# Performance work log

Hardware: AMD Instinct MI355X
Metric: run time of the kernel (lower is better)

The kernel has to match this reference:

```python
import jax, jax.numpy as jnp
import numpy as np

REG_MAX = 16
NUM_CLASSES = 30
IMG_SIZE = 320.0


def make_anchors(strides=(8, 16, 32), feats_shapes=((40, 40), (20, 20), (10, 10))):
    pts = []
    for stride, (h, w) in zip(strides, feats_shapes):
        sx = np.arange(w, dtype=np.float32) + 0.5
        sy = np.arange(h, dtype=np.float32) + 0.5
        gy, gx = np.meshgrid(sy, sx, indexing='ij')
        pts.append(np.stack((gx, gy), -1).reshape(-1, 2) * stride)
    return jnp.asarray(np.concatenate(pts, 0))  # [2100, 2]


def setup_inputs() -> dict:
    key = jax.random.key(0)
    k1, k2, k3, k4 = jax.random.split(key, 4)
    B, M = 128, 50
    pred = jax.random.normal(k1, (B, 4 * REG_MAX + NUM_CLASSES, 2100), dtype=jnp.float32)
    targets_cls = jax.random.randint(k2, (B, M), 0, NUM_CLASSES, dtype=jnp.int32)
    targets_xy = jax.random.uniform(k3, (B, M, 2), dtype=jnp.float32)  # normalized centers
    valid = jax.random.randint(k4, (B, M), 0, 2) > 0  # bool GT-validity mask
    anchors = make_anchors()
    return {"pred": pred, "targets_cls": targets_cls, "targets_xy": targets_xy,
            "valid": valid, "anchors": anchors}


def reference(pred, targets_cls, targets_xy, valid, anchors):
    B = pred.shape[0]
    A = anchors.shape[0]  # 2100
    pred_dist = pred[:, :4 * REG_MAX, :]   # [B, 64, A]
    pred_cls = pred[:, 4 * REG_MAX:, :]    # [B, C, A]

    # --- vectorized nearest-anchor assignment (replaces nested python loops) ---
    centers = targets_xy * IMG_SIZE                               # [B, M, 2]
    dist = jnp.linalg.norm(anchors[None, None, :, :] - centers[:, :, None, :], axis=-1)  # [B, M, A]
    best = jnp.argmin(dist, axis=-1)                              # [B, M]

    b_idx = jnp.broadcast_to(jnp.arange(B)[:, None], best.shape)  # [B, M]
    fg_mask = jnp.zeros((B, A), dtype=bool).at[b_idx, best].max(valid)
    target_cls = jnp.zeros_like(pred_cls).at[b_idx, targets_cls, best].max(
        valid.astype(pred_cls.dtype))

    # --- BCEWithLogits, mean over all elements ---
    loss_cls = jnp.mean(-(target_cls * jax.nn.log_sigmoid(pred_cls)
                          + (1.0 - target_cls) * jax.nn.log_sigmoid(-pred_cls)))

    # --- Huber(delta=1) on pred_dist.mean(dim=1)[fg_mask] vs 1.0, mean over fg ---
    m = pred_dist.mean(axis=1)            # [B, A]
    e = m - 1.0
    huber = jnp.where(jnp.abs(e) <= 1.0, 0.5 * e * e, jnp.abs(e) - 0.5)
    cnt = fg_mask.sum().astype(pred.dtype)
    loss_box = jnp.where(cnt > 0,
                         (huber * fg_mask.astype(pred.dtype)).sum() / jnp.maximum(cnt, 1.0),
                         jnp.zeros((), pred.dtype))
    return (loss_box, loss_cls)
```

## Files before the change

kernel.cpp:

```cpp
#include <hip/hip_runtime.h>
#include <cfloat>
#include <cmath>

#define BB 128
#define MM 50
#define AA 2100
#define NC 30
#define DCH 64
#define CHT 94

__global__ void assign_kernel(const float* __restrict__ txy,
                              const int* __restrict__ tcls,
                              const unsigned char* __restrict__ valid,
                              const float* __restrict__ anchors,
                              unsigned int* __restrict__ mask) {
    int gtid = blockIdx.x * blockDim.x + threadIdx.x;
    int pair = gtid >> 6;
    int lane = gtid & 63;
    if (pair >= BB * MM) return;
    if (!valid[pair]) return;

    float cx = txy[pair * 2 + 0] * 320.0f;
    float cy = txy[pair * 2 + 1] * 320.0f;

    const float2* __restrict__ anc = (const float2*)anchors;
    float bd = FLT_MAX;
    int   bi = 0x7fffffff;
    #pragma unroll 4
    for (int a = lane; a < AA; a += 64) {
        float2 p = anc[a];
        float dx = p.x - cx;
        float dy = p.y - cy;
        float d = dx * dx + dy * dy;
        if (d < bd) { bd = d; bi = a; }
    }
    for (int off = 32; off > 0; off >>= 1) {
        float od = __shfl_xor(bd, off);
        int   oi = __shfl_xor(bi, off);
        if (od < bd || (od == bd && oi < bi)) { bd = od; bi = oi; }
    }
    if (lane == 0) {
        int b = pair / MM;
        int c = tcls[pair];
        atomicOr(&mask[b * AA + bi], (1u << c) | 0x80000000u);
    }
}

__global__ __launch_bounds__(256)
void loss_kernel(const float* __restrict__ pred,
                 const unsigned int* __restrict__ mask,
                 double* __restrict__ sums,
                 unsigned int* __restrict__ cnt) {
    int idx = blockIdx.x * blockDim.x + threadIdx.x;
    float acc_cls = 0.0f;
    float box = 0.0f;
    int is_fg = 0;

    if (idx < BB * AA) {
        int b = idx / AA;
        int a = idx - b * AA;
        const float* __restrict__ pc = pred + (size_t)b * CHT * AA
                                            + (size_t)DCH * AA + a;
        unsigned int mw = mask[idx];

        float x[NC];
        #pragma unroll
        for (int c = 0; c < NC; ++c) x[c] = pc[(size_t)c * AA];

        #pragma unroll
        for (int c = 0; c < NC; ++c) {
            float v = x[c];
            float sp = fmaxf(v, 0.0f) + __logf(1.0f + __expf(-fabsf(v)));
            acc_cls += sp - (((mw >> c) & 1u) ? v : 0.0f);
        }

        if (mw & 0x80000000u) {
            const float* __restrict__ pd = pred + (size_t)b * CHT * AA + a;
            float s = 0.0f;
            #pragma unroll 16
            for (int ch = 0; ch < DCH; ++ch) s += pd[(size_t)ch * AA];
            float m = s * (1.0f / 64.0f);
            float e = m - 1.0f;
            float ae = fabsf(e);
            box = (ae <= 1.0f) ? 0.5f * e * e : ae - 0.5f;
            is_fg = 1;
        }
    }

    for (int off = 32; off > 0; off >>= 1) {
        acc_cls += __shfl_down(acc_cls, off);
        box     += __shfl_down(box, off);
    }
    unsigned long long bal = __ballot(is_fg);

    __shared__ float s_cls[4];
    __shared__ float s_box[4];
    __shared__ unsigned int s_fg[4];
    int lane = threadIdx.x & 63;
    int w    = threadIdx.x >> 6;
    if (lane == 0) {
        s_cls[w] = acc_cls;
        s_box[w] = box;
        s_fg[w]  = (unsigned int)__popcll(bal);
    }
    __syncthreads();
    if (threadIdx.x == 0) {
        double tc = (double)s_cls[0] + s_cls[1] + s_cls[2] + s_cls[3];
        double tb = (double)s_box[0] + s_box[1] + s_box[2] + s_box[3];
        unsigned int tf = s_fg[0] + s_fg[1] + s_fg[2] + s_fg[3];
        atomicAdd(&sums[0], tc);
        atomicAdd(&sums[1], tb);
        if (tf) atomicAdd(cnt, tf);
    }
}

__global__ void finalize_kernel(const double* __restrict__ sums,
                                const unsigned int* __restrict__ cnt,
                                float* __restrict__ out) {
    double sum_cls = sums[0];
    double sum_box = sums[1];
    unsigned int c = *cnt;
    out[0] = (c > 0) ? (float)(sum_box / (double)c) : 0.0f;
    out[1] = (float)(sum_cls / (double)((size_t)BB * NC * AA));
}

extern "C" void kernel_launch(void* const* d_in, const int* in_sizes, int n_in,
                              void* d_out, int out_size, void* d_ws, size_t ws_size,
                              hipStream_t stream) {
    const float*         pred    = (const float*)d_in[0];
    const int*           tcls    = (const int*)d_in[1];
    const float*         txy     = (const float*)d_in[2];
    const unsigned char* valid   = (const unsigned char*)d_in[3];
    const float*         anchors = (const float*)d_in[4];

    float* out = (float*)d_out;

    const size_t MASK_BYTES = (size_t)BB * AA * sizeof(unsigned int);
    unsigned int* mask = (unsigned int*)d_ws;
    double*       sums = (double*)((char*)d_ws + MASK_BYTES);
    unsigned int* cnt  = (unsigned int*)((char*)d_ws + MASK_BYTES + 2 * sizeof(double));

    hipMemsetAsync(d_ws, 0, MASK_BYTES + 2 * sizeof(double) + sizeof(unsigned int), stream);

    {
        int threads = BB * MM * 64;
        int block = 256;
        int grid = (threads + block - 1) / block;
        assign_kernel<<<grid, block, 0, stream>>>(txy, tcls, valid, anchors, mask);
    }
    {
        int total = BB * AA;
        int block = 256;
        int grid = (total + block - 1) / block;
        loss_kernel<<<grid, block, 0, stream>>>(pred, mask, sums, cnt);
    }
    finalize_kernel<<<1, 1, 0, stream>>>(sums, cnt, out);
}
```

Before: 176.2 us.

## Replace dense anchor mask with per-GT codes, vectorize loss, fuse finalize via ticket

The assign kernel now writes a compact per-GT code (anchor index and class) and zeroes the accumulators itself, so the dense B×A mask and its memset are no longer needed. The loss kernel has each thread handle 4 anchors with float4 loads. Each thread rebuilds its mask words by scanning the 50 GT codes of its batch. The separate finalize kernel is replaced by a last-block ticket pattern that writes the outputs. This removes a memset launch, a kernel launch and mask traffic, at the cost of a 50-iteration code scan per thread and fewer threads in flight.

```diff
diff --git a/kernel.cpp b/kernel.cpp
--- a/kernel.cpp
+++ b/kernel.cpp
@@ -8,17 +8,27 @@
 #define NC 30
 #define DCH 64
 #define CHT 94
+#define GPB 525
+#define LOSS_BLOCK 128
+#define LOSS_GRID ((BB * GPB) / LOSS_BLOCK)
 
 __global__ void assign_kernel(const float* __restrict__ txy,
                               const int* __restrict__ tcls,
                               const unsigned char* __restrict__ valid,
                               const float* __restrict__ anchors,
-                              unsigned int* __restrict__ mask) {
+                              unsigned int* __restrict__ codes,
+                              double* __restrict__ sums,
+                              unsigned int* __restrict__ cnt,
+                              unsigned int* __restrict__ ticket) {
     int gtid = blockIdx.x * blockDim.x + threadIdx.x;
+    if (gtid == 0) { sums[0] = 0.0; sums[1] = 0.0; *cnt = 0u; *ticket = 0u; }
     int pair = gtid >> 6;
     int lane = gtid & 63;
     if (pair >= BB * MM) return;
-    if (!valid[pair]) return;
+    if (!valid[pair]) {
+        if (lane == 0) codes[pair] = 0xFFFFFFFFu;
+        return;
+    }
 
     float cx = txy[pair * 2 + 0] * 320.0f;
     float cy = txy[pair * 2 + 1] * 320.0f;
@@ -39,89 +49,111 @@
         int   oi = __shfl_xor(bi, off);
         if (od < bd || (od == bd && oi < bi)) { bd = od; bi = oi; }
     }
-    if (lane == 0) {
-        int b = pair / MM;
-        int c = tcls[pair];
-        atomicOr(&mask[b * AA + bi], (1u << c) | 0x80000000u);
-    }
+    if (lane == 0)
+        codes[pair] = (unsigned int)bi | ((unsigned int)tcls[pair] << 16);
 }
 
-__global__ __launch_bounds__(256)
+__device__ __forceinline__ float huber_of_mean(float s) {
+    float e = s * (1.0f / 64.0f) - 1.0f;
+    float ae = fabsf(e);
+    return (ae <= 1.0f) ? 0.5f * e * e : ae - 0.5f;
+}
+
+__global__ __launch_bounds__(LOSS_BLOCK)
 void loss_kernel(const float* __restrict__ pred,
-                 const unsigned int* __restrict__ mask,
+                 const unsigned int* __restrict__ codes,
                  double* __restrict__ sums,
-                 unsigned int* __restrict__ cnt) {
-    int idx = blockIdx.x * blockDim.x + threadIdx.x;
-    float acc_cls = 0.0f;
-    float box = 0.0f;
-    int is_fg = 0;
+                 unsigned int* __restrict__ cnt,
+                 unsigned int* __restrict__ ticket,
+                 float* __restrict__ out) {
+    int idx = blockIdx.x * LOSS_BLOCK + threadIdx.x;
+    int b = idx / GPB;
+    int g = idx - b * GPB;
+    int a0 = g * 4;
+    const float* __restrict__ pb = pred + (size_t)b * CHT * AA;
 
-    if (idx < BB * AA) {
-        int b = idx / AA;
-        int a = idx - b * AA;
-        const float* __restrict__ pc = pred + (size_t)b * CHT * AA
-                                            + (size_t)DCH * AA + a;
-        unsigned int mw = mask[idx];
+    const float* __restrict__ pc = pb + (size_t)DCH * AA + a0;
+    float4 xs[NC];
+    #pragma unroll
+    for (int c = 0; c < NC; ++c)
+        xs[c] = *(const float4*)(pc + (size_t)c * AA);
 
-        float x[NC];
-        #pragma unroll
-        for (int c = 0; c < NC; ++c) x[c] = pc[(size_t)c * AA];
-
-        #pragma unroll
-        for (int c = 0; c < NC; ++c) {
-            float v = x[c];
-            float sp = fmaxf(v, 0.0f) + __logf(1.0f + __expf(-fabsf(v)));
-            acc_cls += sp - (((mw >> c) & 1u) ? v : 0.0f);
-        }
-
-        if (mw & 0x80000000u) {
-            const float* __restrict__ pd = pred + (size_t)b * CHT * AA + a;
-            float s = 0.0f;
-            #pragma unroll 16
-            for (int ch = 0; ch < DCH; ++ch) s += pd[(size_t)ch * AA];
-            float m = s * (1.0f / 64.0f);
-            float e = m - 1.0f;
-            float ae = fabsf(e);
-            box = (ae <= 1.0f) ? 0.5f * e * e : ae - 0.5f;
-            is_fg = 1;
+    unsigned int mw0 = 0, mw1 = 0, mw2 = 0, mw3 = 0;
+    const unsigned int* __restrict__ cb = codes + b * MM;
+    #pragma unroll 5
+    for (int m = 0; m < MM; ++m) {
+        unsigned int code = cb[m];
+        if (code != 0xFFFFFFFFu) {
+            int best = (int)(code & 0xFFFFu);
+            unsigned int bit = (1u << (code >> 16)) | 0x80000000u;
+            unsigned int d = (unsigned int)(best - a0);
+            if (d < 4u) {
+                if (d == 0u) mw0 |= bit;
+                else if (d == 1u) mw1 |= bit;
+                else if (d == 2u) mw2 |= bit;
+                else mw3 |= bit;
+            }
         }
     }
 
+    float acc = 0.0f;
+    #pragma unroll
+    for (int c = 0; c < NC; ++c) {
+        float4 v = xs[c];
+        float sp;
+        sp = fmaxf(v.x, 0.f) + __logf(1.f + __expf(-fabsf(v.x)));
+        acc += sp - (((mw0 >> c) & 1u) ? v.x : 0.f);
+        sp = fmaxf(v.y, 0.f) + __logf(1.f + __expf(-fabsf(v.y)));
+        acc += sp - (((mw1 >> c) & 1u) ? v.y : 0.f);
+        sp = fmaxf(v.z, 0.f) + __logf(1.f + __expf(-fabsf(v.z)));
+        acc += sp - (((mw2 >> c) & 1u) ? v.z : 0.f);
+        sp = fmaxf(v.w, 0.f) + __logf(1.f + __expf(-fabsf(v.w)));
+        acc += sp - (((mw3 >> c) & 1u) ? v.w : 0.f);
+    }
+
+    float box = 0.0f;
+    unsigned int nfg = 0;
+    if ((mw0 | mw1 | mw2 | mw3) & 0x80000000u) {
+        float4 s = make_float4(0.f, 0.f, 0.f, 0.f);
+        #pragma unroll 8
+        for (int ch = 0; ch < DCH; ++ch) {
+            float4 v = *(const float4*)(pb + (size_t)ch * AA + a0);
+            s.x += v.x; s.y += v.y; s.z += v.z; s.w += v.w;
+        }
+        if (mw0 >> 31) { box += huber_of_mean(s.x); nfg++; }
+        if (mw1 >> 31) { box += huber_of_mean(s.y); nfg++; }
+        if (mw2 >> 31) { box += huber_of_mean(s.z); nfg++; }
+        if (mw3 >> 31) { box += huber_of_mean(s.w); nfg++; }
+    }
+
     for (int off = 32; off > 0; off >>= 1) {
-        acc_cls += __shfl_down(acc_cls, off);
-        box     += __shfl_down(box, off);
+        acc += __shfl_down(acc, off);
+        box += __shfl_down(box, off);
+        nfg += __shfl_down(nfg, off);
     }
-    unsigned long long bal = __ballot(is_fg);
+    __shared__ float s_cls[2];
+    __shared__ float s_box[2];
+    __shared__ unsigned int s_fg[2];
+    int lane = threadIdx.x & 63;
+    int w = threadIdx.x >> 6;
+    if (lane == 0) { s_cls[w] = acc; s_box[w] = box; s_fg[w] = nfg; }
+    __syncthreads();
 
-    __shared__ float s_cls[4];
-    __shared__ float s_box[4];
-    __shared__ unsigned int s_fg[4];
-    int lane = threadIdx.x & 63;
-    int w    = threadIdx.x >> 6;
-    if (lane == 0) {
-        s_cls[w] = acc_cls;
-        s_box[w] = box;
-        s_fg[w]  = (unsigned int)__popcll(bal);
+    if (threadIdx.x == 0) {
+        atomicAdd(&sums[0], (double)((double)s_cls[0] + (double)s_cls[1]));
+        atomicAdd(&sums[1], (double)((double)s_box[0] + (double)s_box[1]));
+        unsigned int tf = s_fg[0] + s_fg[1];
+        if (tf) atomicAdd(cnt, tf);
+        __threadfence();
+        unsigned int old = atomicAdd(ticket, 1u);
+        if (old == (unsigned int)(LOSS_GRID - 1)) {
+            double tc = atomicAdd(&sums[0], 0.0);
+            double tb = atomicAdd(&sums[1], 0.0);
+            unsigned int c = atomicAdd(cnt, 0u);
+            out[0] = (c > 0) ? (float)(tb / (double)c) : 0.0f;
+            out[1] = (float)(tc / (double)((size_t)BB * NC * AA));
+        }
     }
-    __syncthreads();
-    if (threadIdx.x == 0) {
-        double tc = (double)s_cls[0] + s_cls[1] + s_cls[2] + s_cls[3];
-        double tb = (double)s_box[0] + s_box[1] + s_box[2] + s_box[3];
-        unsigned int tf = s_fg[0] + s_fg[1] + s_fg[2] + s_fg[3];
-        atomicAdd(&sums[0], tc);
-        atomicAdd(&sums[1], tb);
-        if (tf) atomicAdd(cnt, tf);
-    }
-}
-
-__global__ void finalize_kernel(const double* __restrict__ sums,
-                                const unsigned int* __restrict__ cnt,
-                                float* __restrict__ out) {
-    double sum_cls = sums[0];
-    double sum_box = sums[1];
-    unsigned int c = *cnt;
-    out[0] = (c > 0) ? (float)(sum_box / (double)c) : 0.0f;
-    out[1] = (float)(sum_cls / (double)((size_t)BB * NC * AA));
 }
 
 extern "C" void kernel_launch(void* const* d_in, const int* in_sizes, int n_in,
@@ -132,27 +164,20 @@
     const float*         txy     = (const float*)d_in[2];
     const unsigned char* valid   = (const unsigned char*)d_in[3];
     const float*         anchors = (const float*)d_in[4];
-
     float* out = (float*)d_out;
 
-    const size_t MASK_BYTES = (size_t)BB * AA * sizeof(unsigned int);
-    unsigned int* mask = (unsigned int*)d_ws;
-    double*       sums = (double*)((char*)d_ws + MASK_BYTES);
-    unsigned int* cnt  = (unsigned int*)((char*)d_ws + MASK_BYTES + 2 * sizeof(double));
-
-    hipMemsetAsync(d_ws, 0, MASK_BYTES + 2 * sizeof(double) + sizeof(unsigned int), stream);
+    double*       sums   = (double*)d_ws;
+    unsigned int* cnt    = (unsigned int*)((char*)d_ws + 16);
+    unsigned int* ticket = (unsigned int*)((char*)d_ws + 20);
+    unsigned int* codes  = (unsigned int*)((char*)d_ws + 24);
 
     {
         int threads = BB * MM * 64;
         int block = 256;
         int grid = (threads + block - 1) / block;
-        assign_kernel<<<grid, block, 0, stream>>>(txy, tcls, valid, anchors, mask);
+        assign_kernel<<<grid, block, 0, stream>>>(txy, tcls, valid, anchors,
+                                                  codes, sums, cnt, ticket);
     }
-    {
-        int total = BB * AA;
-        int block = 256;
-        int grid = (total + block - 1) / block;
-        loss_kernel<<<grid, block, 0, stream>>>(pred, mask, sums, cnt);
-    }
-    finalize_kernel<<<1, 1, 0, stream>>>(sums, cnt, out);
+    loss_kernel<<<LOSS_GRID, LOSS_BLOCK, 0, stream>>>(pred, codes, sums, cnt,
+                                                      ticket, out);
 }
```

Measured after the change: 199.8 us. 1.13x slower.

## Split loss kernel into vectorized BCE blocks and separate sparse box blocks

Applied to the files above, without the earlier changes.

Restructures the loss kernel so most blocks process the 30 class channels with float4 loads over a flattened (class, batch, group) index in a grid-stride loop, while a small set of dedicated blocks scan the mask and compute the Huber term only for foreground anchors. Block partial sums now go to 64 slotted atomics that a 64-thread finalize kernel reduces, instead of every block hitting one pair of global doubles. The aim is wider memory transactions, less atomic contention and keeping the divergent box path out of the BCE wavefronts; the cost is re-reading the mask word once per class and some extra index arithmetic.

```diff
diff --git a/kernel.cpp b/kernel.cpp
--- a/kernel.cpp
+++ b/kernel.cpp
@@ -8,6 +8,15 @@
 #define NC 30
 #define DCH 64
 #define CHT 94
+#define GPB 525
+#define NITEM (NC * BB * GPB)
+#define BLK 256
+#define NBCE 1984
+#define NBOX 64
+#define NGRID (NBCE + NBOX)
+#define NSLOT 64
+
+#define MASK_BYTES (BB * AA * 4)
 
 __global__ void assign_kernel(const float* __restrict__ txy,
                               const int* __restrict__ tcls,
@@ -26,7 +35,7 @@
     const float2* __restrict__ anc = (const float2*)anchors;
     float bd = FLT_MAX;
     int   bi = 0x7fffffff;
-    #pragma unroll 4
+    #pragma unroll 8
     for (int a = lane; a < AA; a += 64) {
         float2 p = anc[a];
         float dx = p.x - cx;
@@ -41,87 +50,100 @@
     }
     if (lane == 0) {
         int b = pair / MM;
-        int c = tcls[pair];
-        atomicOr(&mask[b * AA + bi], (1u << c) | 0x80000000u);
+        atomicOr(&mask[b * AA + bi], (1u << tcls[pair]) | 0x80000000u);
     }
 }
 
-__global__ __launch_bounds__(256)
+__global__ __launch_bounds__(BLK)
 void loss_kernel(const float* __restrict__ pred,
                  const unsigned int* __restrict__ mask,
-                 double* __restrict__ sums,
-                 unsigned int* __restrict__ cnt) {
-    int idx = blockIdx.x * blockDim.x + threadIdx.x;
-    float acc_cls = 0.0f;
+                 double* __restrict__ pcls,
+                 double* __restrict__ pbox,
+                 unsigned int* __restrict__ pcnt) {
+    float acc = 0.0f;
     float box = 0.0f;
-    int is_fg = 0;
+    unsigned int nfg = 0;
 
-    if (idx < BB * AA) {
-        int b = idx / AA;
-        int a = idx - b * AA;
-        const float* __restrict__ pc = pred + (size_t)b * CHT * AA
-                                            + (size_t)DCH * AA + a;
-        unsigned int mw = mask[idx];
-
-        float x[NC];
-        #pragma unroll
-        for (int c = 0; c < NC; ++c) x[c] = pc[(size_t)c * AA];
-
-        #pragma unroll
-        for (int c = 0; c < NC; ++c) {
-            float v = x[c];
-            float sp = fmaxf(v, 0.0f) + __logf(1.0f + __expf(-fabsf(v)));
-            acc_cls += sp - (((mw >> c) & 1u) ? v : 0.0f);
+    if (blockIdx.x < NBCE) {
+        int tid = blockIdx.x * BLK + threadIdx.x;
+        const int stride = NBCE * BLK;
+        for (int item = tid; item < NITEM; item += stride) {
+            int c = item / (BB * GPB);
+            int r = item - c * (BB * GPB);
+            int b = r / GPB;
+            int g = r - b * GPB;
+            float4 v  = *(const float4*)(pred + (size_t)(b * CHT + DCH + c) * AA + g * 4);
+            uint4  mw = *(const uint4*)(mask + b * AA + g * 4);
+            float sp;
+            sp = fmaxf(v.x, 0.f) + __logf(1.f + __expf(-fabsf(v.x)));
+            acc += sp - (((mw.x >> c) & 1u) ? v.x : 0.f);
+            sp = fmaxf(v.y, 0.f) + __logf(1.f + __expf(-fabsf(v.y)));
+            acc += sp - (((mw.y >> c) & 1u) ? v.y : 0.f);
+            sp = fmaxf(v.z, 0.f) + __logf(1.f + __expf(-fabsf(v.z)));
+            acc += sp - (((mw.z >> c) & 1u) ? v.z : 0.f);
+            sp = fmaxf(v.w, 0.f) + __logf(1.f + __expf(-fabsf(v.w)));
+            acc += sp - (((mw.w >> c) & 1u) ? v.w : 0.f);
         }
-
-        if (mw & 0x80000000u) {
-            const float* __restrict__ pd = pred + (size_t)b * CHT * AA + a;
-            float s = 0.0f;
-            #pragma unroll 16
-            for (int ch = 0; ch < DCH; ++ch) s += pd[(size_t)ch * AA];
-            float m = s * (1.0f / 64.0f);
-            float e = m - 1.0f;
-            float ae = fabsf(e);
-            box = (ae <= 1.0f) ? 0.5f * e * e : ae - 0.5f;
-            is_fg = 1;
+    } else {
+        int tid = (blockIdx.x - NBCE) * BLK + threadIdx.x;
+        const int stride = NBOX * BLK;
+        for (int i = tid; i < BB * AA; i += stride) {
+            unsigned int mw = mask[i];
+            if (mw >> 31) {
+                int b = i / AA;
+                int a = i - b * AA;
+                const float* __restrict__ pd = pred + (size_t)b * CHT * AA + a;
+                float s = 0.0f;
+                #pragma unroll 16
+                for (int ch = 0; ch < DCH; ++ch) s += pd[(size_t)ch * AA];
+                float e = s * (1.0f / 64.0f) - 1.0f;
+                float ae = fabsf(e);
+                box += (ae <= 1.0f) ? 0.5f * e * e : ae - 0.5f;
+                nfg++;
+            }
         }
     }
 
     for (int off = 32; off > 0; off >>= 1) {
-        acc_cls += __shfl_down(acc_cls, off);
-        box     += __shfl_down(box, off);
+        acc += __shfl_down(acc, off);
+        box += __shfl_down(box, off);
+        nfg += __shfl_down(nfg, off);
     }
-    unsigned long long bal = __ballot(is_fg);
-
     __shared__ float s_cls[4];
     __shared__ float s_box[4];
     __shared__ unsigned int s_fg[4];
     int lane = threadIdx.x & 63;
     int w    = threadIdx.x >> 6;
-    if (lane == 0) {
-        s_cls[w] = acc_cls;
-        s_box[w] = box;
-        s_fg[w]  = (unsigned int)__popcll(bal);
-    }
+    if (lane == 0) { s_cls[w] = acc; s_box[w] = box; s_fg[w] = nfg; }
     __syncthreads();
     if (threadIdx.x == 0) {
-        double tc = (double)s_cls[0] + s_cls[1] + s_cls[2] + s_cls[3];
-        double tb = (double)s_box[0] + s_box[1] + s_box[2] + s_box[3];
+        int slot = blockIdx.x & (NSLOT - 1);
+        float tc = s_cls[0] + s_cls[1] + s_cls[2] + s_cls[3];
+        float tb = s_box[0] + s_box[1] + s_box[2] + s_box[3];
         unsigned int tf = s_fg[0] + s_fg[1] + s_fg[2] + s_fg[3];
-        atomicAdd(&sums[0], tc);
-        atomicAdd(&sums[1], tb);
-        if (tf) atomicAdd(cnt, tf);
+        atomicAdd(&pcls[slot], (double)tc);
+        if (tb != 0.0f) atomicAdd(&pbox[slot], (double)tb);
+        if (tf)         atomicAdd(&pcnt[slot], tf);
     }
 }
 
-__global__ void finalize_kernel(const double* __restrict__ sums,
-                                const unsigned int* __restrict__ cnt,
+__global__ void finalize_kernel(const double* __restrict__ pcls,
+                                const double* __restrict__ pbox,
+                                const unsigned int* __restrict__ pcnt,
                                 float* __restrict__ out) {
-    double sum_cls = sums[0];
-    double sum_box = sums[1];
-    unsigned int c = *cnt;
-    out[0] = (c > 0) ? (float)(sum_box / (double)c) : 0.0f;
-    out[1] = (float)(sum_cls / (double)((size_t)BB * NC * AA));
+    int t = threadIdx.x;
+    double cs = pcls[t];
+    double bs = pbox[t];
+    unsigned int ct = pcnt[t];
+    for (int off = 32; off > 0; off >>= 1) {
+        cs += __shfl_down(cs, off);
+        bs += __shfl_down(bs, off);
+        ct += __shfl_down(ct, off);
+    }
+    if (t == 0) {
+        out[0] = (ct > 0) ? (float)(bs / (double)ct) : 0.0f;
+        out[1] = (float)(cs / (double)((size_t)BB * NC * AA));
+    }
 }
 
 extern "C" void kernel_launch(void* const* d_in, const int* in_sizes, int n_in,
@@ -132,27 +154,20 @@
     const float*         txy     = (const float*)d_in[2];
     const unsigned char* valid   = (const unsigned char*)d_in[3];
     const float*         anchors = (const float*)d_in[4];
-
     float* out = (float*)d_out;
 
-    const size_t MASK_BYTES = (size_t)BB * AA * sizeof(unsigned int);
     unsigned int* mask = (unsigned int*)d_ws;
-    double*       sums = (double*)((char*)d_ws + MASK_BYTES);
-    unsigned int* cnt  = (unsigned int*)((char*)d_ws + MASK_BYTES + 2 * sizeof(double));
+    double*       pcls = (double*)((char*)d_ws + MASK_BYTES);
+    double*       pbox = (double*)((char*)d_ws + MASK_BYTES + 512);
+    unsigned int* pcnt = (unsigned int*)((char*)d_ws + MASK_BYTES + 1024);
 
-    hipMemsetAsync(d_ws, 0, MASK_BYTES + 2 * sizeof(double) + sizeof(unsigned int), stream);
+    hipMemsetAsync(d_ws, 0, MASK_BYTES + 1280, stream);
 
     {
         int threads = BB * MM * 64;
-        int block = 256;
-        int grid = (threads + block - 1) / block;
-        assign_kernel<<<grid, block, 0, stream>>>(txy, tcls, valid, anchors, mask);
+        int grid = (threads + BLK - 1) / BLK;
+        assign_kernel<<<grid, BLK, 0, stream>>>(txy, tcls, valid, anchors, mask);
     }
-    {
-        int total = BB * AA;
-        int block = 256;
-        int grid = (total + block - 1) / block;
-        loss_kernel<<<grid, block, 0, stream>>>(pred, mask, sums, cnt);
-    }
-    finalize_kernel<<<1, 1, 0, stream>>>(sums, cnt, out);
+    loss_kernel<<<NGRID, BLK, 0, stream>>>(pred, mask, pcls, pbox, pcnt);
+    finalize_kernel<<<1, 64, 0, stream>>>(pcls, pbox, pcnt, out);
 }
```

New measurement: 182.0 us. +3.3%, slower.
